# Kernel tuning notes

Hardware: AMD Instinct MI355X
Metric: run time of the kernel (lower is better)

Reference implementation:

```python
import jax, jax.numpy as jnp
import numpy as np

BATCH = 8
N_CLASSES = 3            # including background
PRE_NMS_LIMIT = 6000
NMS_THRESH = 0.5
SCALE = 512.0
WINDOW = (0.0, 0.0, 512.0, 512.0)   # y1, x1, y2, x2
STD_DEV = np.array([0.1, 0.1, 0.2, 0.2], np.float32)
GROUP_OFFSET = 4096.0    # > image extent; separates (batch, class) groups in NMS

_RATIOS = np.array([0.5, 1.0, 2.0])
_LEVELS = [((128, 128), 4, 8.0), ((64, 64), 8, 16.0), ((32, 32), 16, 32.0), ((16, 16), 32, 64.0)]


def _gen_anchors():
    # faithful port of generate_pyramid_anchors / generate_anchors (anchor_stride=1)
    out = []
    for (fy, fx), stride, scale in _LEVELS:
        s, r = np.meshgrid(np.array([scale]), _RATIOS)
        s, r = s.flatten(), r.flatten()
        heights = s / np.sqrt(r)
        widths = s * np.sqrt(r)
        sy = np.arange(fy) * stride
        sx = np.arange(fx) * stride
        sx, sy = np.meshgrid(sx, sy)
        bw, bcx = np.meshgrid(widths, sx)
        bh, bcy = np.meshgrid(heights, sy)
        centers = np.stack([bcy, bcx], axis=2).reshape(-1, 2)
        sizes = np.stack([bh, bw], axis=2).reshape(-1, 2)
        out.append(np.concatenate([centers - 0.5 * sizes, centers + 0.5 * sizes], axis=1))
    return np.concatenate(out, axis=0).astype(np.float32)  # (65280, 4) yxyx


def setup_inputs() -> dict:
    key = jax.random.key(0)
    k1, k2 = jax.random.split(key)
    anchors = jnp.asarray(_gen_anchors())
    n_anchors = anchors.shape[0]
    n_prop = BATCH * n_anchors
    logits = jax.random.normal(k1, (n_prop, N_CLASSES), jnp.float32)
    probs = jax.nn.softmax(logits, axis=-1)
    deltas = jax.random.normal(k2, (n_prop, 4), jnp.float32)
    batch_ixs = jnp.repeat(jnp.arange(BATCH, dtype=jnp.int64), n_anchors)
    return {"probs": probs, "deltas": deltas, "anchors": anchors, "batch_ixs": batch_ixs}


def _apply_box_deltas_2d(boxes, deltas):
    # boxes: (K,4) yxyx (normalized); deltas: (K,4) dy,dx,dh,dw
    h = boxes[:, 2] - boxes[:, 0]
    w = boxes[:, 3] - boxes[:, 1]
    cy = boxes[:, 0] + 0.5 * h + deltas[:, 0] * h
    cx = boxes[:, 1] + 0.5 * w + deltas[:, 1] * w
    h = h * jnp.exp(deltas[:, 2])
    w = w * jnp.exp(deltas[:, 3])
    y1 = cy - 0.5 * h
    x1 = cx - 0.5 * w
    return jnp.stack([y1, x1, y1 + h, x1 + w], axis=1)


def _nms_keep(boxes, thresh):
    # boxes (K,4), already sorted by score descending; returns bool keep mask.
    y1, x1, y2, x2 = boxes[:, 0], boxes[:, 1], boxes[:, 2], boxes[:, 3]
    areas = (y2 - y1 + 1.0) * (x2 - x1 + 1.0)
    ih = jnp.clip(jnp.minimum(y2[:, None], y2[None, :]) - jnp.maximum(y1[:, None], y1[None, :]) + 1.0, 0.0)
    iw = jnp.clip(jnp.minimum(x2[:, None], x2[None, :]) - jnp.maximum(x1[:, None], x1[None, :]) + 1.0, 0.0)
    inter = ih * iw
    iou = inter / (areas[:, None] + areas[None, :] - inter)  # (K,K)
    K = boxes.shape[0]
    idx = jnp.arange(K)

    def body(i, keep):
        sup = (iou[i] >= thresh) & (idx > i) & keep[i]
        return keep & ~sup

    return jax.lax.fori_loop(0, K, body, jnp.ones((K,), bool))


def reference(probs, deltas, anchors, batch_ixs):
    n_anchors = anchors.shape[0]
    n_fg = probs.shape[1] - 1
    # trim to top pre_nms_limit foreground scores (flat over proposals x fg classes)
    fg = probs[:, 1:].reshape(-1)
    scores, flat_ix = jax.lax.top_k(fg, PRE_NMS_LIMIT)  # sorted descending
    prop_ix = flat_ix // n_fg
    class_ids = flat_ix % n_fg + 1
    b = batch_ixs[prop_ix]
    a = anchors[prop_ix % n_anchors]        # anchors tiled per batch element
    d = deltas[prop_ix] * jnp.asarray(STD_DEV)
    rois = _apply_box_deltas_2d(a / SCALE, d) * SCALE
    lo = jnp.array([WINDOW[0], WINDOW[1], WINDOW[0], WINDOW[1]], rois.dtype)
    hi = jnp.array([WINDOW[2], WINDOW[3], WINDOW[2], WINDOW[3]], rois.dtype)
    rois = jnp.clip(rois, lo, hi)
    # batched per-class NMS: offset boxes so different (batch, class) groups never overlap
    group = (b * (n_fg + 1) + class_ids).astype(rois.dtype) * GROUP_OFFSET
    keep = _nms_keep(rois + group[:, None], NMS_THRESH)
    detections = jnp.concatenate(
        [rois, scores[:, None], keep.astype(rois.dtype)[:, None]], axis=1)  # (K, 6)
    return detections, class_ids, b
```

## Files before the change

### kernel.cpp

```cpp
#include <hip/hip_runtime.h>
#include <math.h>

typedef unsigned int u32;
typedef unsigned short u16;
typedef unsigned long long u64;

#define PRE_NMS 6000
#define NBLK    94
#define KMAX    640
#define MSTRIDE 11
#define MAXW    10
#define MTILE   (MAXW * MAXW)
#define FINEB   8192
#define LOWB    8064
#define NHB     64
#define CANDMAX 16384
#define NGRP    24
#define FLOOR_BITS 0x3F000000u

#define CTR_OFF    0
#define FINEH_OFF  256
#define BCNT_OFF   33024
#define GBITS_OFF  98560
#define ZERO_U32   29248
#define CAND_OFF   116992
#define BOXR_OFF   248064
#define KG_OFF     344320
#define GRANKG_OFF 344576
#define BOXG_OFF   406016
#define AREAG_OFF  651776
#define MASKG_OFF  713216
#define BASE_OFF   2064896

__device__ __forceinline__ u32 bucket_of(u32 bits) {
    if (bits >= FLOOR_BITS) {
        u32 fb = (bits - FLOOR_BITS) >> 10; if (fb > FINEB - 1) fb = FINEB - 1;
        return fb;
    }
    return 8192u + (bits >> 17);
}

__global__ __launch_bounds__(256) void zero_kernel(u32* __restrict__ p) {
    int i = blockIdx.x * 256 + threadIdx.x;
    int stride = gridDim.x * 256;
    for (; i < ZERO_U32; i += stride) p[i] = 0u;
}

__global__ __launch_bounds__(1024) void hist_kernel(const float4* __restrict__ probs4,
                                                    u32* __restrict__ fineh,
                                                    int n_prop) {
    __shared__ u32 hf[FINEB];
    int t = threadIdx.x;
    for (int i = t; i < FINEB; i += 1024) hf[i] = 0u;
    __syncthreads();
    int nq = n_prop >> 2;
    int idx = blockIdx.x * 1024 + t;
    int stride = gridDim.x * 1024;
    for (int q = idx; q < nq; q += stride) {
        float4 a = probs4[3 * q + 0];
        float4 b = probs4[3 * q + 1];
        float4 c = probs4[3 * q + 2];
        float vs[8] = {a.y, a.z, b.x, b.y, b.w, c.x, c.z, c.w};
        #pragma unroll
        for (int e = 0; e < 8; ++e) {
            u32 bits = __float_as_uint(vs[e]);
            if (bits >= FLOOR_BITS) {
                u32 fb = (bits - FLOOR_BITS) >> 10; if (fb >= FINEB) fb = FINEB - 1;
                atomicAdd(&hf[fb], 1u);
            }
        }
    }
    __syncthreads();
    for (int b = t; b < FINEB; b += 1024) {
        u32 v = hf[b];
        if (v) atomicAdd(&fineh[b], v);
    }
}

__global__ __launch_bounds__(1024) void pivot_kernel(const float4* __restrict__ probs4,
                                                     const u32* __restrict__ fineh,
                                                     u32* __restrict__ ctr,
                                                     u32* __restrict__ base,
                                                     int n_prop) {
    __shared__ u32 fh[FINEB];
    __shared__ u32 sd[1024];
    __shared__ u32 hlow[LOWB];
    int t = threadIdx.x;
    for (int b = t; b < FINEB; b += 1024) fh[b] = fineh[b];
    __syncthreads();
    int hi = FINEB - 1 - 8 * t;
    u32 L = 0;
    #pragma unroll
    for (int e = 0; e < 8; ++e) L += fh[hi - e];
    sd[t] = L;
    __syncthreads();
    for (int off = 1; off < 1024; off <<= 1) {
        u32 x = (t >= off) ? sd[t - off] : 0u;
        __syncthreads();
        sd[t] += x;
        __syncthreads();
    }
    u32 incl = sd[t], excl = incl - L;
    u32 fineTotal = sd[1023];
    {
        u32 run = excl;
        #pragma unroll
        for (int e = 0; e < 8; ++e) {
            int fb = hi - e;
            base[fb] = run;
            u32 c = fh[fb];
            if (run < (u32)PRE_NMS && run + c >= (u32)PRE_NMS) {
                ctr[1] = FLOOR_BITS + ((u32)fb << 10);
                u32 m = run + c; if (m > (u32)CANDMAX) m = (u32)CANDMAX;
                ctr[0] = m;
            }
            run += c;
        }
    }
    if (fineTotal >= (u32)PRE_NMS) return;

    u32 rem = (u32)PRE_NMS - fineTotal;
    int nq = n_prop >> 2;
    __syncthreads();
    for (int i = t; i < LOWB; i += 1024) hlow[i] = 0u;
    __syncthreads();
    for (int q = t; q < nq; q += 1024) {
        float4 a = probs4[3 * q + 0];
        float4 b = probs4[3 * q + 1];
        float4 c = probs4[3 * q + 2];
        float vs[8] = {a.y, a.z, b.x, b.y, b.w, c.x, c.z, c.w};
        #pragma unroll
        for (int e = 0; e < 8; ++e) {
            u32 bits = __float_as_uint(vs[e]);
            if (bits < FLOOR_BITS) atomicAdd(&hlow[bits >> 17], 1u);
        }
    }
    __syncthreads();
    for (int b = t; b < FINEB; b += 1024) fh[b] = (b < LOWB) ? hlow[b] : 0u;
    __syncthreads();
    L = 0;
    #pragma unroll
    for (int e = 0; e < 8; ++e) L += fh[hi - e];
    sd[t] = L;
    __syncthreads();
    for (int off = 1; off < 1024; off <<= 1) {
        u32 x = (t >= off) ? sd[t - off] : 0u;
        __syncthreads();
        sd[t] += x;
        __syncthreads();
    }
    incl = sd[t]; excl = incl - L;
    {
        u32 run = excl;
        #pragma unroll
        for (int e = 0; e < 8; ++e) {
            int lb = hi - e;
            base[8192 + lb] = fineTotal + run;
            u32 c = fh[lb];
            if (run < rem && run + c >= rem) {
                ctr[1] = ((u32)lb) << 17;
                u32 m = fineTotal + run + c; if (m > (u32)CANDMAX) m = (u32)CANDMAX;
                ctr[0] = m;
            }
            run += c;
        }
    }
}

__global__ __launch_bounds__(256) void scatter_kernel(const float4* __restrict__ probs4,
                                                      const u32* __restrict__ ctr,
                                                      const u32* __restrict__ base,
                                                      u32* __restrict__ bcnt,
                                                      u64* __restrict__ cand,
                                                      int n_prop) {
    u32 pivot = ctr[1];
    int nq = n_prop >> 2;
    int idx = blockIdx.x * 256 + threadIdx.x;
    int stride = gridDim.x * 256;
    for (int q = idx; q < nq; q += stride) {
        float4 a = probs4[3 * q + 0];
        float4 b = probs4[3 * q + 1];
        float4 c = probs4[3 * q + 2];
        float vs[8] = {a.y, a.z, b.x, b.y, b.w, c.x, c.z, c.w};
        #pragma unroll
        for (int e = 0; e < 8; ++e) {
            u32 bits = __float_as_uint(vs[e]);
            if (bits >= pivot) {
                u32 bk = bucket_of(bits);
                u32 off = atomicAdd(&bcnt[bk], 1u);
                u32 slot = base[bk] + off;
                u32 i = (u32)(8 * q + e);
                if (slot < (u32)CANDMAX) cand[slot] = ((u64)bits << 32) | (u64)(~i);
            }
        }
    }
}

__global__ __launch_bounds__(256) void rankdecode_kernel(const u64* __restrict__ cand,
                                                         const u32* __restrict__ ctr,
                                                         const u32* __restrict__ base,
                                                         const u32* __restrict__ bcnt,
                                                         const float4* __restrict__ deltas4,
                                                         const float4* __restrict__ anchors4,
                                                         float4* __restrict__ boxr,
                                                         u32* __restrict__ gbits,
                                                         float* __restrict__ out,
                                                         int n_anch) {
    u32 M = ctr[0]; if (M > (u32)CANDMAX) M = (u32)CANDMAX;
    u32 i = blockIdx.x * 256 + threadIdx.x;
    if (i >= M) return;
    u64 key = cand[i];
    u32 bits = (u32)(key >> 32);
    u32 bk = bucket_of(bits);
    u32 b0 = base[bk];
    u32 n = bcnt[bk];
    u32 r = b0;
    if (n > 1) {
        u32 end = b0 + n; if (end > M) end = M;
        u32 cnt = 0;
        for (u32 j = b0; j < end; ++j) cnt += (cand[j] > key) ? 1u : 0u;
        r = b0 + cnt;
    }
    if (r >= (u32)PRE_NMS) return;
    u32 flat = ~((u32)key);
    int p = (int)(flat >> 1);
    int cls = (int)(flat & 1u) + 1;
    int b = p / n_anch;
    int g = b * 3 + cls;
    int aidx = p - b * n_anch;
    float score = __uint_as_float(bits);
    float4 a = anchors4[aidx];
    float4 d = deltas4[p];
    float d0 = d.x * 0.1f, d1 = d.y * 0.1f, d2 = d.z * 0.2f, d3 = d.w * 0.2f;
    float y1 = a.x * (1.0f / 512.0f), x1 = a.y * (1.0f / 512.0f);
    float y2 = a.z * (1.0f / 512.0f), x2 = a.w * (1.0f / 512.0f);
    float h = y2 - y1, w = x2 - x1;
    float cy = y1 + 0.5f * h + d0 * h;
    float cx = x1 + 0.5f * w + d1 * w;
    h = h * expf(d2);
    w = w * expf(d3);
    float ry1 = (cy - 0.5f * h) * 512.0f;
    float rx1 = (cx - 0.5f * w) * 512.0f;
    float ry2 = (cy - 0.5f * h + h) * 512.0f;
    float rx2 = (cx - 0.5f * w + w) * 512.0f;
    ry1 = fminf(fmaxf(ry1, 0.0f), 512.0f);
    rx1 = fminf(fmaxf(rx1, 0.0f), 512.0f);
    ry2 = fminf(fmaxf(ry2, 0.0f), 512.0f);
    rx2 = fminf(fmaxf(rx2, 0.0f), 512.0f);
    out[r * 6 + 0] = ry1;
    out[r * 6 + 1] = rx1;
    out[r * 6 + 2] = ry2;
    out[r * 6 + 3] = rx2;
    out[r * 6 + 4] = score;
    out[r * 6 + 5] = 1.0f;
    out[PRE_NMS * 6 + r] = (float)cls;
    out[PRE_NMS * 7 + r] = (float)b;
    boxr[r] = make_float4(ry1, rx1, ry2, rx2);
    atomicOr(&gbits[g * 192 + (r >> 5)], 1u << (r & 31));
}

__global__ __launch_bounds__(512) void prep_kernel(const u32* __restrict__ gbits,
                                                   const float4* __restrict__ boxr,
                                                   u32* __restrict__ kg,
                                                   u32* __restrict__ grankg,
                                                   float4* __restrict__ boxg,
                                                   float* __restrict__ areag) {
    __shared__ int bpre[96];
    __shared__ u16 grankS[KMAX];
    __shared__ int sK;
    int g = blockIdx.x, t = threadIdx.x, lane = t & 63, wv = t >> 6;
    const u32* rb32 = gbits + g * 192;

    if (t < 64) {
        u64 w0 = (u64)rb32[2 * lane] | ((u64)rb32[2 * lane + 1] << 32);
        u64 w1 = (lane < NBLK - 64)
                 ? ((u64)rb32[128 + 2 * lane] | ((u64)rb32[129 + 2 * lane] << 32)) : 0ull;
        int c0 = (int)__popcll(w0), c1 = (int)__popcll(w1);
        int i0 = c0, i1 = c1;
        #pragma unroll
        for (int off = 1; off < 64; off <<= 1) {
            int a = __shfl_up(i0, off); if (lane >= off) i0 += a;
            int b = __shfl_up(i1, off); if (lane >= off) i1 += b;
        }
        int tot0 = __shfl(i0, 63), tot1 = __shfl(i1, 63);
        bpre[lane] = i0 - c0;
        if (lane < 32) bpre[64 + lane] = tot0 + ((lane < NBLK - 64) ? (i1 - c1) : 0);
        if (lane == 0) { sK = tot0 + tot1; kg[g] = (u32)(tot0 + tot1); }
    }
    __syncthreads();
    int K = sK;
    if (K == 0) return;
    int Kc = (K < KMAX) ? K : KMAX;

    for (int blk = wv; blk < NBLK; blk += 8) {
        u64 wmask = (u64)rb32[2 * blk] | ((u64)rb32[2 * blk + 1] << 32);
        if ((wmask >> lane) & 1ull) {
            int pos = bpre[blk] + (int)__popcll(wmask & ((1ull << lane) - 1ull));
            if (pos < KMAX) grankS[pos] = (u16)((blk << 6) | lane);
        }
    }
    __syncthreads();

    float4* bg = boxg + g * KMAX;
    float*  ag = areag + g * KMAX;
    u32*    gr = grankg + g * KMAX;
    for (int m = t; m < KMAX; m += 512) {
        if (m < Kc) {
            int r = grankS[m];
            float4 bb = boxr[r];
            bg[m] = bb;
            ag[m] = (bb.z - bb.x + 1.0f) * (bb.w - bb.y + 1.0f);
            gr[m] = (u32)r;
        } else {
            bg[m] = make_float4(-3e30f, -3e30f, -3e30f, -3e30f);
            ag[m] = 3e38f;
        }
    }
}

__global__ __launch_bounds__(64) void mask_kernel(const u32* __restrict__ kg,
                                                  const float4* __restrict__ boxg,
                                                  const float* __restrict__ areag,
                                                  u64* __restrict__ maskg) {
    int g = blockIdx.y;
    u32 K = kg[g];
    if (K == 0u) return;
    int Kc = (K < (u32)KMAX) ? (int)K : KMAX;
    int W = (Kc + 63) >> 6;
    int u = blockIdx.x;
    int c = u / MAXW, rbk = u % MAXW;
    if (c >= W || rbk >= W) return;
    int lane = threadIdx.x;
    int r = rbk * 64 + lane;
    u64* mg = maskg + (size_t)g * (KMAX * MSTRIDE);
    if (rbk > c) { mg[r * MSTRIDE + c] = 0ull; return; }
    int j0 = c << 6;
    const float4* bg = boxg + g * KMAX;
    const float*  ag = areag + g * KMAX;
    float4 rb = bg[r];
    float  ra = ag[r];
    float4 cb = bg[j0 + lane];
    float  ca = ag[j0 + lane];
    u64 word = 0ull;
    #pragma unroll 8
    for (int q = 0; q < 64; ++q) {
        float cbx = __shfl(cb.x, q);
        float cby = __shfl(cb.y, q);
        float cbz = __shfl(cb.z, q);
        float cbw = __shfl(cb.w, q);
        float cav = __shfl(ca, q);
        float ih = fminf(rb.z, cbz) - fmaxf(rb.x, cbx) + 1.0f;
        float iw = fminf(rb.w, cbw) - fmaxf(rb.y, cby) + 1.0f;
        ih = fmaxf(ih, 0.0f); iw = fmaxf(iw, 0.0f);
        bool o = (3.0f * ih * iw >= ra + cav) && ((j0 + q) > r);
        if (o) word |= (1ull << q);
    }
    mg[r * MSTRIDE + c] = word;
}

__global__ __launch_bounds__(512) void greedy_kernel(const u32* __restrict__ kg,
                                                     const u32* __restrict__ grankg,
                                                     const u64* __restrict__ maskg,
                                                     float* __restrict__ out) {
    __shared__ u64 maskm[KMAX * MSTRIDE + 64];
    __shared__ u16 grank[KMAX];
    int g = blockIdx.x, t = threadIdx.x, lane = t & 63;
    u32 K = kg[g];
    if (K == 0u) return;
    int Kc = (K < (u32)KMAX) ? (int)K : KMAX;
    int W = (Kc + 63) >> 6;
    const u64* mg = maskg + (size_t)g * (KMAX * MSTRIDE);
    int nw = Kc * MSTRIDE;
    for (int m = t; m < nw; m += 512) maskm[m] = mg[m];
    for (int m = nw + t; m < nw + 64; m += 512) maskm[m] = 0ull;
    for (int m = t; m < Kc; m += 512) grank[m] = (u16)grankg[g * KMAX + m];
    __syncthreads();

    if (t >= 64) return;
    u64 remv = 0ull;
    for (int w = 0; w < W; ++w) {
        int r0 = w << 6;
        int rend = Kc - r0; if (rend > 64) rend = 64;
        u64 curw = __shfl(remv, w);
        u64 kb = 0ull;
        for (int b0 = 0; b0 < rend; b0 += 8) {
            int n = rend - b0; if (n > 8) n = 8;
            u64 mrow[8], dg[8];
            #pragma unroll
            for (int j = 0; j < 8; ++j) {
                int rr = r0 + b0 + ((j < n) ? j : 0);
                mrow[j] = maskm[rr * MSTRIDE + lane];
                dg[j]   = maskm[rr * MSTRIDE + w];
            }
            #pragma unroll
            for (int j = 0; j < 8; ++j) {
                if (j < n) {
                    int b = b0 + j;
                    u64 km = ((curw >> b) & 1ull) ? 0ull : ~0ull;
                    curw |= dg[j] & km;
                    remv |= mrow[j] & km;
                    kb |= km & (1ull << b);
                }
            }
        }
        if (lane < rend)
            out[(int)grank[r0 + lane] * 6 + 5] = ((kb >> lane) & 1ull) ? 1.0f : 0.0f;
    }
}

extern "C" void kernel_launch(void* const* d_in, const int* in_sizes, int n_in,
                              void* d_out, int out_size, void* d_ws, size_t ws_size,
                              hipStream_t stream) {
    const float*  probs    = (const float*)d_in[0];
    const float4* deltas4  = (const float4*)d_in[1];
    const float4* anchors4 = (const float4*)d_in[2];
    int n_prop = in_sizes[1] / 4;
    int n_anch = in_sizes[2] / 4;

    char* ws = (char*)d_ws;
    u32* ctr      = (u32*)(ws + CTR_OFF);
    u32* fineh    = (u32*)(ws + FINEH_OFF);
    u32* bcnt     = (u32*)(ws + BCNT_OFF);
    u32* gbits    = (u32*)(ws + GBITS_OFF);
    u64* cand     = (u64*)(ws + CAND_OFF);
    float4* boxr  = (float4*)(ws + BOXR_OFF);
    u32* kg       = (u32*)(ws + KG_OFF);
    u32* grankg   = (u32*)(ws + GRANKG_OFF);
    float4* boxg  = (float4*)(ws + BOXG_OFF);
    float* areag  = (float*)(ws + AREAG_OFF);
    u64* maskg    = (u64*)(ws + MASKG_OFF);
    u32* base     = (u32*)(ws + BASE_OFF);
    float* out    = (float*)d_out;

    zero_kernel<<<64, 256, 0, stream>>>((u32*)ws);
    hist_kernel<<<NHB, 1024, 0, stream>>>((const float4*)probs, fineh, n_prop);
    pivot_kernel<<<1, 1024, 0, stream>>>((const float4*)probs, fineh, ctr, base, n_prop);
    scatter_kernel<<<256, 256, 0, stream>>>((const float4*)probs, ctr, base, bcnt,
                                            cand, n_prop);
    rankdecode_kernel<<<CANDMAX / 256, 256, 0, stream>>>(cand, ctr, base, bcnt,
                                                         deltas4, anchors4,
                                                         boxr, gbits, out, n_anch);
    prep_kernel<<<NGRP, 512, 0, stream>>>(gbits, boxr, kg, grankg, boxg, areag);
    mask_kernel<<<dim3(MTILE, NGRP), 64, 0, stream>>>(kg, boxg, areag, maskg);
    greedy_kernel<<<NGRP, 512, 0, stream>>>(kg, grankg, maskg, out);
}
```

Measured before the change: 137.6 us.

## Fold group compaction prep kernel into mask and greedy NMS kernels

Removes the separate prep kernel that compacted per-group box lists, areas and rank arrays into global memory. Each mask tile block now recomputes the group prefix scan from the bitmask and gathers only the row and column ranks it needs, reading boxes directly and computing areas inline. The greedy kernel rebuilds the rank table itself. This saves one launch and a global round trip, at the cost of redundant prefix scans across many mask blocks and a serial bit-walk loop.

```diff
diff --git a/kernel.cpp b/kernel.cpp
--- a/kernel.cpp
+++ b/kernel.cpp
@@ -25,12 +25,8 @@
 #define ZERO_U32   29248
 #define CAND_OFF   116992
 #define BOXR_OFF   248064
-#define KG_OFF     344320
-#define GRANKG_OFF 344576
-#define BOXG_OFF   406016
-#define AREAG_OFF  651776
-#define MASKG_OFF  713216
-#define BASE_OFF   2064896
+#define MASKG_OFF  344320
+#define BASE_OFF   1696000
 
 __device__ __forceinline__ u32 bucket_of(u32 bits) {
     if (bits >= FLOOR_BITS) {
@@ -259,88 +255,100 @@
     atomicOr(&gbits[g * 192 + (r >> 5)], 1u << (r & 31));
 }
 
-__global__ __launch_bounds__(512) void prep_kernel(const u32* __restrict__ gbits,
-                                                   const float4* __restrict__ boxr,
-                                                   u32* __restrict__ kg,
-                                                   u32* __restrict__ grankg,
-                                                   float4* __restrict__ boxg,
-                                                   float* __restrict__ areag) {
+__global__ __launch_bounds__(64) void mask_kernel(const u32* __restrict__ gbits,
+                                                  const float4* __restrict__ boxr,
+                                                  u64* __restrict__ maskg) {
     __shared__ int bpre[96];
-    __shared__ u16 grankS[KMAX];
-    __shared__ int sK;
-    int g = blockIdx.x, t = threadIdx.x, lane = t & 63, wv = t >> 6;
+    __shared__ u16 rowRank[64];
+    __shared__ u16 colRank[64];
+    int g = blockIdx.y;
+    int lane = threadIdx.x;
     const u32* rb32 = gbits + g * 192;
 
-    if (t < 64) {
-        u64 w0 = (u64)rb32[2 * lane] | ((u64)rb32[2 * lane + 1] << 32);
-        u64 w1 = (lane < NBLK - 64)
-                 ? ((u64)rb32[128 + 2 * lane] | ((u64)rb32[129 + 2 * lane] << 32)) : 0ull;
-        int c0 = (int)__popcll(w0), c1 = (int)__popcll(w1);
-        int i0 = c0, i1 = c1;
-        #pragma unroll
-        for (int off = 1; off < 64; off <<= 1) {
-            int a = __shfl_up(i0, off); if (lane >= off) i0 += a;
-            int b = __shfl_up(i1, off); if (lane >= off) i1 += b;
-        }
-        int tot0 = __shfl(i0, 63), tot1 = __shfl(i1, 63);
-        bpre[lane] = i0 - c0;
-        if (lane < 32) bpre[64 + lane] = tot0 + ((lane < NBLK - 64) ? (i1 - c1) : 0);
-        if (lane == 0) { sK = tot0 + tot1; kg[g] = (u32)(tot0 + tot1); }
-    }
-    __syncthreads();
-    int K = sK;
+    u64 w0 = (u64)rb32[2 * lane] | ((u64)rb32[2 * lane + 1] << 32);
+    u64 w1 = (lane < NBLK - 64)
+             ? ((u64)rb32[128 + 2 * lane] | ((u64)rb32[129 + 2 * lane] << 32)) : 0ull;
+    int c0 = (int)__popcll(w0), c1 = (int)__popcll(w1);
+    int i0 = c0, i1 = c1;
+    #pragma unroll
+    for (int off = 1; off < 64; off <<= 1) {
+        int a = __shfl_up(i0, off); if (lane >= off) i0 += a;
+        int b = __shfl_up(i1, off); if (lane >= off) i1 += b;
+    }
+    int tot0 = __shfl(i0, 63), tot1 = __shfl(i1, 63);
+    bpre[lane] = i0 - c0;
+    if (lane < 32) bpre[64 + lane] = tot0 + ((lane < NBLK - 64) ? (i1 - c1) : 0);
+    int K = tot0 + tot1;
     if (K == 0) return;
     int Kc = (K < KMAX) ? K : KMAX;
-
-    for (int blk = wv; blk < NBLK; blk += 8) {
-        u64 wmask = (u64)rb32[2 * blk] | ((u64)rb32[2 * blk + 1] << 32);
-        if ((wmask >> lane) & 1ull) {
-            int pos = bpre[blk] + (int)__popcll(wmask & ((1ull << lane) - 1ull));
-            if (pos < KMAX) grankS[pos] = (u16)((blk << 6) | lane);
-        }
-    }
-    __syncthreads();
-
-    float4* bg = boxg + g * KMAX;
-    float*  ag = areag + g * KMAX;
-    u32*    gr = grankg + g * KMAX;
-    for (int m = t; m < KMAX; m += 512) {
-        if (m < Kc) {
-            int r = grankS[m];
-            float4 bb = boxr[r];
-            bg[m] = bb;
-            ag[m] = (bb.z - bb.x + 1.0f) * (bb.w - bb.y + 1.0f);
-            gr[m] = (u32)r;
-        } else {
-            bg[m] = make_float4(-3e30f, -3e30f, -3e30f, -3e30f);
-            ag[m] = 3e38f;
-        }
-    }
-}
-
-__global__ __launch_bounds__(64) void mask_kernel(const u32* __restrict__ kg,
-                                                  const float4* __restrict__ boxg,
-                                                  const float* __restrict__ areag,
-                                                  u64* __restrict__ maskg) {
-    int g = blockIdx.y;
-    u32 K = kg[g];
-    if (K == 0u) return;
-    int Kc = (K < (u32)KMAX) ? (int)K : KMAX;
     int W = (Kc + 63) >> 6;
     int u = blockIdx.x;
     int c = u / MAXW, rbk = u % MAXW;
     if (c >= W || rbk >= W) return;
-    int lane = threadIdx.x;
+    u64* mg = maskg + (size_t)g * (KMAX * MSTRIDE);
     int r = rbk * 64 + lane;
-    u64* mg = maskg + (size_t)g * (KMAX * MSTRIDE);
     if (rbk > c) { mg[r * MSTRIDE + c] = 0ull; return; }
     int j0 = c << 6;
-    const float4* bg = boxg + g * KMAX;
-    const float*  ag = areag + g * KMAX;
-    float4 rb = bg[r];
-    float  ra = ag[r];
-    float4 cb = bg[j0 + lane];
-    float  ca = ag[j0 + lane];
+    int rowS = rbk << 6;
+    __syncthreads();
+
+    {
+        int rE = rowS + 64, cE = j0 + 64;
+        int blk = lane;
+        u64 wm = w0;
+        int bb = bpre[blk];
+        int pc = c0;
+        if (!((bb >= rE || bb + pc <= rowS) && (bb >= cE || bb + pc <= j0))) {
+            int pos = bb;
+            while (wm) {
+                int bit = __ffsll((long long)wm) - 1;
+                wm &= wm - 1ull;
+                int rr = pos - rowS;
+                if (rr >= 0 && rr < 64) rowRank[rr] = (u16)((blk << 6) | bit);
+                int cc = pos - j0;
+                if (cc >= 0 && cc < 64) colRank[cc] = (u16)((blk << 6) | bit);
+                ++pos;
+                if (pos >= cE && pos >= rE) break;
+            }
+        }
+        if (lane < NBLK - 64) {
+            blk = 64 + lane;
+            wm = w1;
+            bb = bpre[blk];
+            pc = c1;
+            if (!((bb >= rE || bb + pc <= rowS) && (bb >= cE || bb + pc <= j0))) {
+                int pos = bb;
+                while (wm) {
+                    int bit = __ffsll((long long)wm) - 1;
+                    wm &= wm - 1ull;
+                    int rr = pos - rowS;
+                    if (rr >= 0 && rr < 64) rowRank[rr] = (u16)((blk << 6) | bit);
+                    int cc = pos - j0;
+                    if (cc >= 0 && cc < 64) colRank[cc] = (u16)((blk << 6) | bit);
+                    ++pos;
+                    if (pos >= cE && pos >= rE) break;
+                }
+            }
+        }
+    }
+    __syncthreads();
+
+    float4 rb, cb;
+    float ra, ca;
+    if (r < Kc) {
+        rb = boxr[rowRank[lane]];
+        ra = (rb.z - rb.x + 1.0f) * (rb.w - rb.y + 1.0f);
+    } else {
+        rb = make_float4(-3e30f, -3e30f, -3e30f, -3e30f);
+        ra = 3e38f;
+    }
+    if (j0 + lane < Kc) {
+        cb = boxr[colRank[lane]];
+        ca = (cb.z - cb.x + 1.0f) * (cb.w - cb.y + 1.0f);
+    } else {
+        cb = make_float4(-3e30f, -3e30f, -3e30f, -3e30f);
+        ca = 3e38f;
+    }
     u64 word = 0ull;
     #pragma unroll 8
     for (int q = 0; q < 64; ++q) {
@@ -358,22 +366,49 @@
     mg[r * MSTRIDE + c] = word;
 }
 
-__global__ __launch_bounds__(512) void greedy_kernel(const u32* __restrict__ kg,
-                                                     const u32* __restrict__ grankg,
+__global__ __launch_bounds__(512) void greedy_kernel(const u32* __restrict__ gbits,
                                                      const u64* __restrict__ maskg,
                                                      float* __restrict__ out) {
     __shared__ u64 maskm[KMAX * MSTRIDE + 64];
     __shared__ u16 grank[KMAX];
-    int g = blockIdx.x, t = threadIdx.x, lane = t & 63;
-    u32 K = kg[g];
-    if (K == 0u) return;
-    int Kc = (K < (u32)KMAX) ? (int)K : KMAX;
+    __shared__ int bpre[96];
+    __shared__ int sK;
+    int g = blockIdx.x, t = threadIdx.x, lane = t & 63, wv = t >> 6;
+    const u32* rb32 = gbits + g * 192;
+
+    if (t < 64) {
+        u64 w0 = (u64)rb32[2 * lane] | ((u64)rb32[2 * lane + 1] << 32);
+        u64 w1 = (lane < NBLK - 64)
+                 ? ((u64)rb32[128 + 2 * lane] | ((u64)rb32[129 + 2 * lane] << 32)) : 0ull;
+        int c0 = (int)__popcll(w0), c1 = (int)__popcll(w1);
+        int i0 = c0, i1 = c1;
+        #pragma unroll
+        for (int off = 1; off < 64; off <<= 1) {
+            int a = __shfl_up(i0, off); if (lane >= off) i0 += a;
+            int b = __shfl_up(i1, off); if (lane >= off) i1 += b;
+        }
+        int tot0 = __shfl(i0, 63), tot1 = __shfl(i1, 63);
+        bpre[lane] = i0 - c0;
+        if (lane < 32) bpre[64 + lane] = tot0 + ((lane < NBLK - 64) ? (i1 - c1) : 0);
+        if (lane == 0) sK = tot0 + tot1;
+    }
+    __syncthreads();
+    int K = sK;
+    if (K == 0) return;
+    int Kc = (K < KMAX) ? K : KMAX;
     int W = (Kc + 63) >> 6;
+
+    for (int blk = wv; blk < NBLK; blk += 8) {
+        u64 wmask = (u64)rb32[2 * blk] | ((u64)rb32[2 * blk + 1] << 32);
+        if ((wmask >> lane) & 1ull) {
+            int pos = bpre[blk] + (int)__popcll(wmask & ((1ull << lane) - 1ull));
+            if (pos < KMAX) grank[pos] = (u16)((blk << 6) | lane);
+        }
+    }
     const u64* mg = maskg + (size_t)g * (KMAX * MSTRIDE);
     int nw = Kc * MSTRIDE;
     for (int m = t; m < nw; m += 512) maskm[m] = mg[m];
     for (int m = nw + t; m < nw + 64; m += 512) maskm[m] = 0ull;
-    for (int m = t; m < Kc; m += 512) grank[m] = (u16)grankg[g * KMAX + m];
     __syncthreads();
 
     if (t >= 64) return;
@@ -424,10 +459,6 @@
     u32* gbits    = (u32*)(ws + GBITS_OFF);
     u64* cand     = (u64*)(ws + CAND_OFF);
     float4* boxr  = (float4*)(ws + BOXR_OFF);
-    u32* kg       = (u32*)(ws + KG_OFF);
-    u32* grankg   = (u32*)(ws + GRANKG_OFF);
-    float4* boxg  = (float4*)(ws + BOXG_OFF);
-    float* areag  = (float*)(ws + AREAG_OFF);
     u64* maskg    = (u64*)(ws + MASKG_OFF);
     u32* base     = (u32*)(ws + BASE_OFF);
     float* out    = (float*)d_out;
@@ -440,7 +471,6 @@
     rankdecode_kernel<<<CANDMAX / 256, 256, 0, stream>>>(cand, ctr, base, bcnt,
                                                          deltas4, anchors4,
                                                          boxr, gbits, out, n_anch);
-    prep_kernel<<<NGRP, 512, 0, stream>>>(gbits, boxr, kg, grankg, boxg, areag);
-    mask_kernel<<<dim3(MTILE, NGRP), 64, 0, stream>>>(kg, boxg, areag, maskg);
-    greedy_kernel<<<NGRP, 512, 0, stream>>>(kg, grankg, maskg, out);
-}
+    mask_kernel<<<dim3(MTILE, NGRP), 64, 0, stream>>>(gbits, boxr, maskg);
+    greedy_kernel<<<NGRP, 512, 0, stream>>>(gbits, maskg, out);
+}
```

After: 137.2 us, median of 2. About the same (-0.3%).
